# Performance work log

Measured on AMD Instinct MI355X. Metric: run time of the kernel, lower is better.

## Reference

```python
import jax, jax.numpy as jnp
import numpy as np

GROUP_SIZE = 128
IN_FEATURES = 4096
OUT_FEATURES = 11008
BATCH = 16


def setup_inputs() -> dict:
    key = jax.random.key(0)
    k_x, k_q, k_s, k_z, k_b = jax.random.split(key, 5)
    num_groups = IN_FEATURES // GROUP_SIZE
    x = jax.random.normal(k_x, (BATCH, IN_FEATURES), dtype=jnp.float32)
    # packed int4 pairs stored as bytes in [0, 256)
    qweight = jax.random.randint(k_q, (OUT_FEATURES, IN_FEATURES // 2), 0, 256, dtype=jnp.int32)
    # positive scales of realistic magnitude, zeros in [0, 15]
    scales = jax.random.uniform(k_s, (OUT_FEATURES, num_groups), dtype=jnp.float32) * 0.01 + 1e-4
    zeros = jax.random.uniform(k_z, (OUT_FEATURES, num_groups), dtype=jnp.float32) * 15.0
    bias = jax.random.normal(k_b, (OUT_FEATURES,), dtype=jnp.float32)
    return {"x": x, "qweight": qweight, "scales": scales, "zeros": zeros, "bias": bias}


def _unpack_int4(packed, in_features):
    # packed: [O, I//2] ints in [0,256); low nibble is even column, high nibble odd
    low = packed & 15
    high = (packed >> 4) & 15
    return jnp.stack([low, high], axis=-1).reshape(packed.shape[0], in_features)  # [O, I]


def reference(x, qweight, scales, zeros, bias):
    q = _unpack_int4(qweight, IN_FEATURES).astype(jnp.float32)        # [O, I]
    s = jnp.repeat(scales, GROUP_SIZE, axis=1)                        # [O, I]
    z = jnp.repeat(zeros, GROUP_SIZE, axis=1)                         # [O, I]
    w = (q - z) * s                                                   # dequantized weight [O, I]
    return x @ w.T + bias                                             # [B, O]
```

## Files before the change

### kernel.cpp

```cpp
#include <hip/hip_runtime.h>
#include <hip/hip_fp16.h>

#define IN_F   4096
#define OUT_F  11008
#define BATCH  16
#define GROUPS 32
#define PACKED_PER_ROW (IN_F / 2)

typedef __attribute__((ext_vector_type(8))) _Float16 half8;
typedef __attribute__((ext_vector_type(4))) _Float16 half4;
typedef __attribute__((ext_vector_type(2))) _Float16 h2;
typedef __attribute__((ext_vector_type(4))) float    float4_t;
typedef __attribute__((ext_vector_type(4))) int      int4_t;
typedef __attribute__((ext_vector_type(4))) unsigned uint4_t;

__device__ inline h2 cvt2(float a, float b) {
    return __builtin_bit_cast(h2, __builtin_amdgcn_cvt_pkrtz(a, b));
}

__global__ __launch_bounds__(256) void xcvt(const float* __restrict__ x,
                                            _Float16* __restrict__ xh) {
    const int i = (blockIdx.x * 256 + threadIdx.x) * 4;
    const float4_t v = *(const float4_t*)(x + i);
    half4 h;
    h2 lo = cvt2(v.x, v.y), hi = cvt2(v.z, v.w);
    h[0] = lo[0]; h[1] = lo[1]; h[2] = hi[0]; h[3] = hi[1];
    *(half4*)(xh + i) = h;
}

__global__ __launch_bounds__(64) void gptq_gemm_w(
    const _Float16* __restrict__ xh, const int* __restrict__ qw,
    const float* __restrict__ scales, const float* __restrict__ zeros,
    float* __restrict__ ws_part)
{
    const int lane  = threadIdx.x;
    const int otile = blockIdx.x >> 2;
    const int kq    = blockIdx.x & 3;

    const int ln = lane & 15;
    const int lk = lane >> 4;
    const int o  = otile * 16 + ln;

    const int*      qbase = qw + o * PACKED_PER_ROW + kq * 512 + lk * 4;
    const _Float16* xbase = xh + ln * IN_F + kq * 1024 + lk * 8;

    const float4_t sf0 = *(const float4_t*)(scales + o * GROUPS + kq * 8);
    const float4_t sf1 = *(const float4_t*)(scales + o * GROUPS + kq * 8 + 4);
    const float4_t zf0 = *(const float4_t*)(zeros  + o * GROUPS + kq * 8);
    const float4_t zf1 = *(const float4_t*)(zeros  + o * GROUPS + kq * 8 + 4);
    const float sArr[8] = { sf0.x, sf0.y, sf0.z, sf0.w, sf1.x, sf1.y, sf1.z, sf1.w };
    const float zArr[8] = { zf0.x, zf0.y, zf0.z, zf0.w, zf1.x, zf1.y, zf1.z, zf1.w };

    int4_t qv[2][8];
    half8  xv[2][8];

    #pragma unroll
    for (int t = 0; t < 8; ++t) {
        qv[0][t] = *(const int4_t*)(qbase + t * 16);
        xv[0][t] = *(const half8*)(xbase + t * 32);
    }

    float4_t acc = {0.f, 0.f, 0.f, 0.f};
    const h2 k1024 = { (_Float16)1024.0f, (_Float16)1024.0f };

    #pragma unroll
    for (int c = 0; c < 4; ++c) {
        const int cur = c & 1, nxt = cur ^ 1;
        if (c < 3) {
            #pragma unroll
            for (int t = 0; t < 8; ++t) {
                qv[nxt][t] = *(const int4_t*)(qbase + (c + 1) * 128 + t * 16);
                xv[nxt][t] = *(const half8*)(xbase + (c + 1) * 256 + t * 32);
            }
        }
        h2 s2[2], c2[2];
        #pragma unroll
        for (int gi = 0; gi < 2; ++gi) {
            const float s  = sArr[2 * c + gi];
            const float c0 = -zArr[2 * c + gi] * s;
            s2[gi] = cvt2(s, s);
            c2[gi] = cvt2(c0, c0);
        }
        #pragma unroll
        for (int t = 0; t < 8; ++t) {
            const int gi = t >> 2;
            uint4_t bw;
            #pragma unroll
            for (int i = 0; i < 4; ++i) {
                const unsigned pv = (unsigned)qv[cur][t][i];
                const unsigned u = (pv & 0xFu) | ((pv << 12) & 0xF0000u)
                                 | 0x64006400u;
                h2 q = __builtin_bit_cast(h2, u) - k1024;
                h2 w = q * s2[gi] + c2[gi];
                bw[i] = __builtin_bit_cast(unsigned, w);
            }
            acc = __builtin_amdgcn_mfma_f32_16x16x32_f16(
                xv[cur][t], __builtin_bit_cast(half8, bw), acc, 0, 0, 0);
        }
    }

    #pragma unroll
    for (int r = 0; r < 4; ++r)
        ws_part[(kq * BATCH + lk * 4 + r) * OUT_F + otile * 16 + ln] = acc[r];
}

__global__ __launch_bounds__(256) void gptq_reduce(
    const float* __restrict__ ws_part, const float* __restrict__ bias,
    float* __restrict__ out)
{
    const int idx = blockIdx.x * 256 + threadIdx.x;
    if (idx >= BATCH * OUT_F) return;
    const int o = idx % OUT_F;
    out[idx] = bias[o]
             + ws_part[idx]
             + ws_part[1 * (BATCH * OUT_F) + idx]
             + ws_part[2 * (BATCH * OUT_F) + idx]
             + ws_part[3 * (BATCH * OUT_F) + idx];
}

__global__ __launch_bounds__(256) void gptq_gemm_fb(
    const float* __restrict__ x, const int* __restrict__ qw,
    const float* __restrict__ scales, const float* __restrict__ zeros,
    const float* __restrict__ bias, float* __restrict__ out)
{
    const int tid  = threadIdx.x;
    const int lane = tid & 63;
    const int wave = tid >> 6;
    const int otile = blockIdx.x;
    const int ln = lane & 15, lk = lane >> 4;
    const int o = otile * 16 + ln;
    const int kc0 = wave * 1024;

    const int* qbase = qw + o * PACKED_PER_ROW + (kc0 >> 1) + lk * 4;
    const float* srow = scales + o * GROUPS;
    const float* zrow = zeros  + o * GROUPS;

    float4_t acc = {0.f, 0.f, 0.f, 0.f};
    const h2 k1024 = { (_Float16)1024.0f, (_Float16)1024.0f };

    #pragma unroll
    for (int ch = 0; ch < 4; ++ch) {
        const int cc = kc0 + ch * 256;
        h2 s2[2], c2[2];
        #pragma unroll
        for (int gi = 0; gi < 2; ++gi) {
            const float s  = srow[(cc >> 7) + gi];
            const float c0 = -zrow[(cc >> 7) + gi] * s;
            s2[gi] = cvt2(s, s); c2[gi] = cvt2(c0, c0);
        }
        #pragma unroll
        for (int t = 0; t < 8; ++t) {
            const int4_t v = *(const int4_t*)(qbase + ch * 128 + t * 16);
            const float* xp = x + ln * IN_F + cc + t * 32 + lk * 8;
            const float4_t a0 = *(const float4_t*)(xp);
            const float4_t a1 = *(const float4_t*)(xp + 4);
            half8 af;
            h2 p0 = cvt2(a0.x, a0.y), p1 = cvt2(a0.z, a0.w);
            h2 p2 = cvt2(a1.x, a1.y), p3 = cvt2(a1.z, a1.w);
            af[0]=p0[0]; af[1]=p0[1]; af[2]=p1[0]; af[3]=p1[1];
            af[4]=p2[0]; af[5]=p2[1]; af[6]=p3[0]; af[7]=p3[1];
            const int gi = t >> 2;
            uint4_t bw;
            #pragma unroll
            for (int i = 0; i < 4; ++i) {
                const unsigned pv = (unsigned)v[i];
                const unsigned u = (pv & 0xFu) | ((pv << 12) & 0xF0000u)
                                 | 0x64006400u;
                h2 q = __builtin_bit_cast(h2, u) - k1024;
                h2 w = q * s2[gi] + c2[gi];
                bw[i] = __builtin_bit_cast(unsigned, w);
            }
            acc = __builtin_amdgcn_mfma_f32_16x16x32_f16(
                af, __builtin_bit_cast(half8, bw), acc, 0, 0, 0);
        }
    }

    __shared__ float red[4][16][17];
    #pragma unroll
    for (int r = 0; r < 4; ++r) red[wave][lk * 4 + r][ln] = acc[r];
    __syncthreads();
    const int row = tid >> 4, col = tid & 15;
    const float sum = red[0][row][col] + red[1][row][col]
                    + red[2][row][col] + red[3][row][col];
    const int oo = otile * 16 + col;
    out[row * OUT_F + oo] = sum + bias[oo];
}

extern "C" void kernel_launch(void* const* d_in, const int* in_sizes, int n_in,
                              void* d_out, int out_size, void* d_ws, size_t ws_size,
                              hipStream_t stream) {
    const float* x      = (const float*)d_in[0];
    const int*   qwgt   = (const int*)d_in[1];
    const float* scales = (const float*)d_in[2];
    const float* zeros  = (const float*)d_in[3];
    const float* bias   = (const float*)d_in[4];
    float* out = (float*)d_out;

    const int nOTiles = OUT_F / 16;
    const size_t need = (size_t)8 << 20;

    if (d_ws && ws_size >= need) {
        float*    ws_part = (float*)d_ws;
        _Float16* xh      = (_Float16*)((char*)d_ws + (4 << 20));
        hipLaunchKernelGGL(xcvt, dim3(BATCH * IN_F / 1024), dim3(256), 0, stream,
                           x, xh);
        hipLaunchKernelGGL(gptq_gemm_w, dim3(nOTiles * 4), dim3(64), 0, stream,
                           xh, qwgt, scales, zeros, ws_part);
        hipLaunchKernelGGL(gptq_reduce, dim3((BATCH * OUT_F + 255) / 256),
                           dim3(256), 0, stream, ws_part, bias, out);
    } else {
        hipLaunchKernelGGL(gptq_gemm_fb, dim3(nOTiles), dim3(256), 0, stream,
                           x, qwgt, scales, zeros, bias, out);
    }
}
```

Before: 35.30 us.

## Hand-schedule weight and activation loads with inline asm and explicit vmcnt waits

Replaces the compiler-scheduled double-buffered loads in the main GEMM kernel with inline-asm global_load_dwordx4 instructions that use immediate offsets. The first two chunks are issued up front, and explicit s_waitcnt vmcnt(16) fences ensure only the chunk being computed has landed. This keeps about two chunks of loads in flight per wave to hide memory latency. It also precomputes all eight group scale and offset pairs before the main loop. The risk is that the compiler cannot see these asynchronous loads, so correctness depends on the manual waitcnt placement and on register allocation not clobbering in-flight destinations.

```diff
diff --git a/kernel.cpp b/kernel.cpp
--- a/kernel.cpp
+++ b/kernel.cpp
@@ -41,8 +41,8 @@
     const int lk = lane >> 4;
     const int o  = otile * 16 + ln;
 
-    const int*      qbase = qw + o * PACKED_PER_ROW + kq * 512 + lk * 4;
-    const _Float16* xbase = xh + ln * IN_F + kq * 1024 + lk * 8;
+    const int*      qaddr = qw + o * PACKED_PER_ROW + kq * 512 + lk * 4;
+    const _Float16* xaddr = xh + ln * IN_F + kq * 1024 + lk * 8;
 
     const float4_t sf0 = *(const float4_t*)(scales + o * GROUPS + kq * 8);
     const float4_t sf1 = *(const float4_t*)(scales + o * GROUPS + kq * 8 + 4);
@@ -50,58 +50,81 @@
     const float4_t zf1 = *(const float4_t*)(zeros  + o * GROUPS + kq * 8 + 4);
     const float sArr[8] = { sf0.x, sf0.y, sf0.z, sf0.w, sf1.x, sf1.y, sf1.z, sf1.w };
     const float zArr[8] = { zf0.x, zf0.y, zf0.z, zf0.w, zf1.x, zf1.y, zf1.z, zf1.w };
+    h2 s2g[8], c2g[8];
+    #pragma unroll
+    for (int gi = 0; gi < 8; ++gi) {
+        const float s  = sArr[gi];
+        const float c0 = -zArr[gi] * s;
+        s2g[gi] = cvt2(s, s);
+        c2g[gi] = cvt2(c0, c0);
+    }
 
     int4_t qv[2][8];
     half8  xv[2][8];
-
-    #pragma unroll
-    for (int t = 0; t < 8; ++t) {
-        qv[0][t] = *(const int4_t*)(qbase + t * 16);
-        xv[0][t] = *(const half8*)(xbase + t * 32);
-    }
+    const h2 k1024 = { (_Float16)1024.0f, (_Float16)1024.0f };
+
+#define GLQ(B,T,OFF) asm volatile("global_load_dwordx4 %0, %1, off offset:%2" \
+                                  : "=v"(qv[B][T]) : "v"(qaddr), "n"(OFF));
+#define GLX(B,T,OFF) asm volatile("global_load_dwordx4 %0, %1, off offset:%2" \
+                                  : "=v"(xv[B][T]) : "v"(xaddr), "n"(OFF));
+#define LOAD_CHUNK(B, CB) \
+    GLQ(B,0,CB+0)   GLX(B,0,CB+0)   GLQ(B,1,CB+64)  GLX(B,1,CB+64)  \
+    GLQ(B,2,CB+128) GLX(B,2,CB+128) GLQ(B,3,CB+192) GLX(B,3,CB+192) \
+    GLQ(B,4,CB+256) GLX(B,4,CB+256) GLQ(B,5,CB+320) GLX(B,5,CB+320) \
+    GLQ(B,6,CB+384) GLX(B,6,CB+384) GLQ(B,7,CB+448) GLX(B,7,CB+448)
+
+#define VWAIT16 { asm volatile("s_waitcnt vmcnt(16)" ::: "memory"); \
+                  __builtin_amdgcn_sched_barrier(0); }
+#define VWAIT0  { asm volatile("s_waitcnt vmcnt(0)"  ::: "memory"); \
+                  __builtin_amdgcn_sched_barrier(0); }
+
+#define COMPUTE(B, C) { \
+    _Pragma("unroll") \
+    for (int t = 0; t < 8; ++t) { \
+        const int gi = 2*(C) + (t >> 2); \
+        uint4_t bw; \
+        _Pragma("unroll") \
+        for (int i = 0; i < 4; ++i) { \
+            const unsigned pv = (unsigned)qv[B][t][i]; \
+            const unsigned u = (pv & 0xFu) | ((pv << 12) & 0xF0000u) \
+                             | 0x64006400u;              \
+            h2 q = __builtin_bit_cast(h2, u) - k1024;    \
+            h2 w = q * s2g[gi] + c2g[gi];                \
+            bw[i] = __builtin_bit_cast(unsigned, w); \
+        } \
+        acc = __builtin_amdgcn_mfma_f32_16x16x32_f16( \
+            xv[B][t], __builtin_bit_cast(half8, bw), acc, 0, 0, 0); \
+    } }
 
     float4_t acc = {0.f, 0.f, 0.f, 0.f};
-    const h2 k1024 = { (_Float16)1024.0f, (_Float16)1024.0f };
-
-    #pragma unroll
-    for (int c = 0; c < 4; ++c) {
-        const int cur = c & 1, nxt = cur ^ 1;
-        if (c < 3) {
-            #pragma unroll
-            for (int t = 0; t < 8; ++t) {
-                qv[nxt][t] = *(const int4_t*)(qbase + (c + 1) * 128 + t * 16);
-                xv[nxt][t] = *(const half8*)(xbase + (c + 1) * 256 + t * 32);
-            }
-        }
-        h2 s2[2], c2[2];
-        #pragma unroll
-        for (int gi = 0; gi < 2; ++gi) {
-            const float s  = sArr[2 * c + gi];
-            const float c0 = -zArr[2 * c + gi] * s;
-            s2[gi] = cvt2(s, s);
-            c2[gi] = cvt2(c0, c0);
-        }
-        #pragma unroll
-        for (int t = 0; t < 8; ++t) {
-            const int gi = t >> 2;
-            uint4_t bw;
-            #pragma unroll
-            for (int i = 0; i < 4; ++i) {
-                const unsigned pv = (unsigned)qv[cur][t][i];
-                const unsigned u = (pv & 0xFu) | ((pv << 12) & 0xF0000u)
-                                 | 0x64006400u;
-                h2 q = __builtin_bit_cast(h2, u) - k1024;
-                h2 w = q * s2[gi] + c2[gi];
-                bw[i] = __builtin_bit_cast(unsigned, w);
-            }
-            acc = __builtin_amdgcn_mfma_f32_16x16x32_f16(
-                xv[cur][t], __builtin_bit_cast(half8, bw), acc, 0, 0, 0);
-        }
-    }
+
+    LOAD_CHUNK(0, 0)
+    LOAD_CHUNK(1, 512)
+
+    VWAIT16
+    COMPUTE(0, 0)
+    LOAD_CHUNK(0, 1024)
+
+    VWAIT16
+    COMPUTE(1, 1)
+    LOAD_CHUNK(1, 1536)
+
+    VWAIT16
+    COMPUTE(0, 2)
+
+    VWAIT0
+    COMPUTE(1, 3)
 
     #pragma unroll
     for (int r = 0; r < 4; ++r)
         ws_part[(kq * BATCH + lk * 4 + r) * OUT_F + otile * 16 + ln] = acc[r];
+
+#undef GLQ
+#undef GLX
+#undef LOAD_CHUNK
+#undef VWAIT16
+#undef VWAIT0
+#undef COMPUTE
 }
 
 __global__ __launch_bounds__(256) void gptq_reduce(
```

Result: no change. 35.19 us (-0.3%).
